# Kernel optimization log

Hardware: AMD Instinct MI355X
Metric: run time of the kernel (lower is better)

Reference implementation:

```python
import jax, jax.numpy as jnp
import numpy as np

N, HID, EDGE_DIM, E = 512, 16, 8, 8192
H4 = HID * 4


def _mlp(x, params):
    W0, b0, W1, b1, W2, b2, W3, b3 = params
    h = jax.nn.relu(x @ W0 + b0)
    h = jax.nn.relu(h @ W1 + b1)
    h = jax.nn.relu(h @ W2 + b2)
    return h @ W3 + b3


def setup_inputs() -> dict:
    key = jax.random.key(0)
    ks = jax.random.split(key, 16)
    rng = np.random.default_rng(0)
    flat = rng.choice(N * N, size=E, replace=False)  # unique edges -> add == set
    edge_index = jnp.asarray(np.stack([flat // N, flat % N]), dtype=jnp.int32)

    def lin(k, fan_in, fan_out):
        kw, kb = jax.random.split(k)
        s = 1.0 / np.sqrt(fan_in)
        return (jax.random.uniform(kw, (fan_in, fan_out), jnp.float32, -s, s),
                jax.random.uniform(kb, (fan_out,), jnp.float32, -s, s))

    W0, b0 = lin(ks[0], EDGE_DIM, H4)
    W1, b1 = lin(ks[1], H4, H4)
    W2, b2 = lin(ks[2], H4, H4)
    W3, b3 = lin(ks[3], H4, HID * HID)
    V0, c0 = lin(ks[4], HID, H4)
    V1, c1 = lin(ks[5], H4, H4)
    V2, c2 = lin(ks[6], H4, H4)
    V3, c3 = lin(ks[7], H4, HID)
    L, Lb = lin(ks[8], HID, HID)

    return {
        'mtr': jax.random.normal(ks[9], (N, N, HID), jnp.float32),
        'edge_attr': jax.random.normal(ks[10], (E, EDGE_DIM), jnp.float32),
        'edge_index': edge_index,
        'W0': W0, 'b0': b0, 'W1': W1, 'b1': b1, 'W2': W2, 'b2': b2, 'W3': W3, 'b3': b3,
        'V0': V0, 'c0': c0, 'V1': V1, 'c1': c1, 'V2': V2, 'c2': c2, 'V3': V3, 'c3': c3,
        'L': L, 'Lb': Lb,
    }


def reference(mtr, edge_attr, edge_index,
              W0, b0, W1, b1, W2, b2, W3, b3,
              V0, c0, V1, c1, V2, c2, V3, c3,
              L, Lb):
    n, hid = mtr.shape[0], mtr.shape[2]
    src, dst = edge_index[0], edge_index[1]
    # per-edge hid x hid matrices (edge_fc)
    F = _mlp(edge_attr, (W0, b0, W1, b1, W2, b2, W3, b3)).reshape(-1, hid, hid)
    # sparse form of einsum('ijc,jkct->ikt', mtr, fmtr): gather src column,
    # per-edge matmul, scatter-add into dst column (edges unique -> == dense set)
    msg = jnp.einsum('iec,ect->iet', mtr[:, src, :], F)          # [n, E, hid]
    mtr1 = jax.ops.segment_sum(msg.transpose(1, 0, 2), dst, num_segments=n)  # [k, i, t]
    mtr1 = mtr1.transpose(1, 0, 2)                                # [i, k, t]
    idx = jnp.arange(n)
    mtr1 = mtr1.at[idx, idx, :].set(0.0)
    mtr1 = mtr1 / hid
    trans = mtr1.transpose(1, 0, 2) @ L + Lb                      # linear(mtr1^T)
    return mtr + _mlp(mtr1 + trans, (V0, c0, V1, c1, V2, c2, V3, c3))
```

## Files before the change

kernel.cpp:

```cpp
#include <hip/hip_runtime.h>
#include <hip/hip_bf16.h>

#define NN 512
#define EE 8192

#define OFF_F     0u
#define OFF_MTR1  2097152u
#define OFF_W     6291456u
#define WR_W0   0
#define WR_B0   512
#define WR_W1   576
#define WR_B1   4672
#define WR_W2   4736
#define WR_B2   8832
#define WR_W3   8896
#define WR_B3   25280
#define WR_V0T  25536
#define WR_C0   26560
#define WR_V1   26624
#define WR_C1   30720
#define WR_V2   30784
#define WR_C2   34880
#define WR_V3   34944
#define WR_C3   35968
#define WR_L    35984
#define WR_LB   36240
#define W_TOTAL 36256
#define OFF_OFFS    (OFF_W + W_TOTAL)
#define OFF_SORTED  (OFF_OFFS + 513)
#define OFF_FLAG    (OFF_SORTED + EE)
#define OFF_MTRT    6336420u
#define OFF_OFFSP   8433572u
#define OFF_SORTEDP 8434085u
#define OFF_FPACK   8442792u
#define OFF_VPACK   9491496u
#define WS_NEED_BYTES  ((size_t)(OFF_MTRT  + 2097152u) * 4u)
#define WS_FULL_BYTES  ((size_t)(OFF_FPACK + 1048704u) * 4u)
#define WS_FULL2_BYTES ((size_t)(OFF_VPACK + 5632u) * 4u)

#define VP0OFF 0
#define VP1OFF 2048
#define VP2OFF 6144
#define VP3OFF 10240

#define XSTR 72
#define RSTR 20

typedef __attribute__((ext_vector_type(8))) short bf16x8;
typedef __attribute__((ext_vector_type(4))) float f32x4;

__device__ __forceinline__ float bflo(unsigned u){ return __uint_as_float(u << 16); }
__device__ __forceinline__ float bfhi(unsigned u){ return __uint_as_float(u & 0xffff0000u); }
__device__ __forceinline__ unsigned short f2bf(float f){
  __hip_bfloat16 h = __float2bfloat16(f);
  union { __hip_bfloat16 hh; unsigned short ss; } u;
  u.hh = h; return u.ss;
}
__device__ __forceinline__ unsigned pack2(float a, float b){
  return (unsigned)f2bf(a) | ((unsigned)f2bf(b) << 16);
}

__device__ __forceinline__ void load16f(const void* base, size_t eoff, int f32, float m[16]) {
  if (f32) {
    const float4* p = (const float4*)((const float*)base + eoff);
    float4 a = p[0], b = p[1], c = p[2], d = p[3];
    m[0]=a.x; m[1]=a.y; m[2]=a.z; m[3]=a.w;
    m[4]=b.x; m[5]=b.y; m[6]=b.z; m[7]=b.w;
    m[8]=c.x; m[9]=c.y; m[10]=c.z; m[11]=c.w;
    m[12]=d.x; m[13]=d.y; m[14]=d.z; m[15]=d.w;
  } else {
    const uint4* p = (const uint4*)((const __hip_bfloat16*)base + eoff);
    uint4 u0 = p[0], u1 = p[1];
    m[0]=bflo(u0.x);  m[1]=bfhi(u0.x);  m[2]=bflo(u0.y);  m[3]=bfhi(u0.y);
    m[4]=bflo(u0.z);  m[5]=bfhi(u0.z);  m[6]=bflo(u0.w);  m[7]=bfhi(u0.w);
    m[8]=bflo(u1.x);  m[9]=bfhi(u1.x);  m[10]=bflo(u1.y); m[11]=bfhi(u1.y);
    m[12]=bflo(u1.z); m[13]=bfhi(u1.z); m[14]=bflo(u1.w); m[15]=bfhi(u1.w);
  }
}

__device__ __forceinline__ float ldelem(const void* p, int idx, int f32) {
  return f32 ? ((const float*)p)[idx]
             : __bfloat162float(((const __hip_bfloat16*)p)[idx]);
}

__global__ void prep_weights(
  const void* __restrict__ W0, const void* __restrict__ b0,
  const void* __restrict__ W1, const void* __restrict__ b1,
  const void* __restrict__ W2, const void* __restrict__ b2,
  const void* __restrict__ W3, const void* __restrict__ b3,
  const void* __restrict__ V0, const void* __restrict__ c0,
  const void* __restrict__ V1, const void* __restrict__ c1,
  const void* __restrict__ V2, const void* __restrict__ c2,
  const void* __restrict__ V3, const void* __restrict__ c3,
  const void* __restrict__ L,  const void* __restrict__ Lb,
  const unsigned short* __restrict__ mtr_u16,
  int* __restrict__ flag, float* __restrict__ w)
{
  __shared__ float mx[256];
  int tid = threadIdx.x;
  float m = 0.f;
  for (int t = tid; t < 4096; t += 256) {
    float v = __uint_as_float(((unsigned)mtr_u16[t]) << 16);
    if (v != v) m = 3e38f;
    else m = fmaxf(m, fabsf(v));
  }
  mx[tid] = m;
  __syncthreads();
  for (int s = 128; s > 0; s >>= 1) {
    if (tid < s) mx[tid] = fmaxf(mx[tid], mx[tid + s]);
    __syncthreads();
  }
  const int f32 = (mx[0] > 1e6f) ? 1 : 0;
  if (blockIdx.x == 0 && tid == 0) flag[0] = f32;

  int g = blockIdx.x * blockDim.x + tid;
  int stride = gridDim.x * blockDim.x;
  auto cv = [&](const void* p, int off, int n){
    for (int i = g; i < n; i += stride) w[off + i] = ldelem(p, i, f32);
  };
  cv(W0, WR_W0, 512);  cv(b0, WR_B0, 64);
  cv(W1, WR_W1, 4096); cv(b1, WR_B1, 64);
  cv(W2, WR_W2, 4096); cv(b2, WR_B2, 64);
  cv(W3, WR_W3, 16384);cv(b3, WR_B3, 256);
  for (int idx = g; idx < 1024; idx += stride) {
    int j = idx >> 4, t = idx & 15;
    w[WR_V0T + idx] = ldelem(V0, t * 64 + j, f32);
  }
  cv(c0, WR_C0, 64);
  cv(V1, WR_V1, 4096); cv(c1, WR_C1, 64);
  cv(V2, WR_V2, 4096); cv(c2, WR_C2, 64);
  cv(V3, WR_V3, 1024); cv(c3, WR_C3, 16);
  cv(L,  WR_L,  256);  cv(Lb, WR_LB, 16);
}

__global__ void prep_vpack(const float* __restrict__ w, unsigned short* __restrict__ VP)
{
  int g = blockIdx.x * blockDim.x + threadIdx.x;
  int stride = gridDim.x * blockDim.x;
  for (int idx = g; idx < 2048; idx += stride) {
    int j = idx & 7, lp = (idx >> 3) & 63, nt = idx >> 9;
    int nn = lp & 15, qq = lp >> 4;
    int kk = qq * 8 + j;
    float v = (kk < 16) ? w[WR_V0T + (nt * 16 + nn) * 16 + kk] : 0.f;
    VP[VP0OFF + idx] = f2bf(v);
  }
  for (int idx = g; idx < 4096; idx += stride) {
    int j = idx & 7, lp = (idx >> 3) & 63, tile = idx >> 9;
    int nn = lp & 15, qq = lp >> 4;
    int kc = tile >> 2, nt = tile & 3;
    int kk = kc * 32 + qq * 8 + j;
    VP[VP1OFF + idx] = f2bf(w[WR_V1 + kk * 64 + nt * 16 + nn]);
    VP[VP2OFF + idx] = f2bf(w[WR_V2 + kk * 64 + nt * 16 + nn]);
  }
  for (int idx = g; idx < 1024; idx += stride) {
    int j = idx & 7, lp = (idx >> 3) & 63, kc = idx >> 9;
    int nn = lp & 15, qq = lp >> 4;
    int kk = kc * 32 + qq * 8 + j;
    VP[VP3OFF + idx] = f2bf(w[WR_V3 + kk * 16 + nn]);
  }
}

__global__ void build_bins(const int* __restrict__ ei,
                           int* __restrict__ offs, int* __restrict__ sorted,
                           int* __restrict__ offsP, int* __restrict__ sortedP,
                           unsigned short* __restrict__ Fpack, int write_pack)
{
  __shared__ int cnt[512];
  __shared__ int pcs[512];
  __shared__ int cur[512];
  __shared__ int curP[512];
  int tid = threadIdx.x;
  cnt[tid] = 0;
  __syncthreads();
  for (int e = tid; e < EE; e += 512) atomicAdd(&cnt[ei[EE + e]], 1);
  __syncthreads();
  int myc = cnt[tid];
  int myp = (myc + 1) & ~1;
  pcs[tid] = myp;
  __syncthreads();
  for (int off = 1; off < 512; off <<= 1) {
    int a = 0, b = 0;
    if (tid >= off) { a = cnt[tid - off]; b = pcs[tid - off]; }
    __syncthreads();
    cnt[tid] += a; pcs[tid] += b;
    __syncthreads();
  }
  int exc  = cnt[tid] - myc;
  int excP = pcs[tid] - myp;
  offs[tid]  = exc;
  offsP[tid] = excP;
  if (tid == 511) { offs[512] = cnt[511]; offsP[512] = pcs[511]; }
  cur[tid]  = exc;
  curP[tid] = excP;
  if (myc & 1) sortedP[excP + myc] = EE;
  __syncthreads();
  for (int e = tid; e < EE; e += 512) {
    int d = ei[EE + e];
    sorted[atomicAdd(&cur[d], 1)]   = e;
    sortedP[atomicAdd(&curP[d], 1)] = e;
  }
  if (write_pack) {
    unsigned* fz = (unsigned*)(Fpack + (size_t)EE * 256);
    for (int idx = tid; idx < 128; idx += 512) fz[idx] = 0u;
  }
}

__global__ __launch_bounds__(256) void transpose_mtr(
  const void* __restrict__ mtr, const int* __restrict__ flag,
  __hip_bfloat16* __restrict__ mtrT)
{
  const int f32 = flag[0];
  int s = blockIdx.x;
  int i = blockIdx.y * 256 + threadIdx.x;
  float m[16];
  load16f(mtr, (size_t)i * 8192 + (size_t)s * 16, f32, m);
  unsigned pw[8];
  #pragma unroll
  for (int q = 0; q < 8; q++) pw[q] = pack2(m[2*q], m[2*q+1]);
  uint4* op = (uint4*)(mtrT + (size_t)s * 8192 + (size_t)i * 16);
  op[0] = make_uint4(pw[0], pw[1], pw[2], pw[3]);
  op[1] = make_uint4(pw[4], pw[5], pw[6], pw[7]);
}

__global__ __launch_bounds__(256) void edge_mlp(
  const void* __restrict__ ea, const float* __restrict__ w,
  const int* __restrict__ flag, float* __restrict__ Fws,
  unsigned short* __restrict__ Fpack, int write_pack)
{
  const int f32 = flag[0];
  const float* W0f = w + WR_W0; const float* b0f = w + WR_B0;
  const float* W1f = w + WR_W1; const float* b1f = w + WR_B1;
  const float* W2f = w + WR_W2; const float* b2f = w + WR_B2;
  const float* W3f = w + WR_W3; const float* b3f = w + WR_B3;
  int tid = threadIdx.x;
  int eg = tid >> 6, lane = tid & 63;
  int e = blockIdx.x * 4 + eg;
  __shared__ float shA[4][64];
  __shared__ float shB[4][64];

  float x[8];
  if (f32) {
    const float4* p = (const float4*)((const float*)ea + (size_t)e * 8);
    float4 a = p[0], b = p[1];
    x[0]=a.x; x[1]=a.y; x[2]=a.z; x[3]=a.w;
    x[4]=b.x; x[5]=b.y; x[6]=b.z; x[7]=b.w;
  } else {
    uint4 u = *(const uint4*)((const __hip_bfloat16*)ea + (size_t)e * 8);
    x[0]=bflo(u.x); x[1]=bfhi(u.x); x[2]=bflo(u.y); x[3]=bfhi(u.y);
    x[4]=bflo(u.z); x[5]=bfhi(u.z); x[6]=bflo(u.w); x[7]=bfhi(u.w);
  }

  float s = b0f[lane];
  #pragma unroll
  for (int c = 0; c < 8; c++) s += x[c] * W0f[c * 64 + lane];
  shA[eg][lane] = fmaxf(s, 0.f);
  __syncthreads();

  s = b1f[lane];
  #pragma unroll
  for (int c = 0; c < 64; c++) s += shA[eg][c] * W1f[c * 64 + lane];
  shB[eg][lane] = fmaxf(s, 0.f);
  __syncthreads();

  s = b2f[lane];
  #pragma unroll
  for (int c = 0; c < 64; c++) s += shB[eg][c] * W2f[c * 64 + lane];
  shA[eg][lane] = fmaxf(s, 0.f);
  __syncthreads();

  int quad = lane >> 4, tt = lane & 15;
  #pragma unroll
  for (int r = 0; r < 4; r++) {
    int o = r * 64 + lane;
    float t = b3f[o];
    #pragma unroll
    for (int c = 0; c < 64; c++) t += shA[eg][c] * W3f[c * 256 + o];
    Fws[(size_t)e * 256 + o] = t;
    if (write_pack) {
      int cc = r * 4 + quad;
      Fpack[(size_t)e * 256 + (cc >> 3) * 128 + tt * 8 + (cc & 7)] = f2bf(t);
    }
  }
}

__global__ __launch_bounds__(256) void message_mfma(
  const __hip_bfloat16* __restrict__ mtrT, const int* __restrict__ ei,
  const unsigned short* __restrict__ Fpack, const int* __restrict__ offsP,
  const int* __restrict__ sortedP, float* __restrict__ mtr1T)
{
  int k = blockIdx.x;
  int tid = threadIdx.x;
  int wave = tid >> 6, lane = tid & 63;
  int n = lane & 15, quad = lane >> 4;
  int qh = quad >> 1;
  int qq = quad & 1;
  int ibase = blockIdx.y * 256 + wave * 64;
  int j0 = offsP[k], j1 = offsP[k + 1];

  f32x4 acc[4];
  #pragma unroll
  for (int mt = 0; mt < 4; mt++) acc[mt] = (f32x4){0.f, 0.f, 0.f, 0.f};

  for (int j = j0; j < j1; j += 2) {
    int e1 = __builtin_amdgcn_readfirstlane(sortedP[j]);
    int e2 = __builtin_amdgcn_readfirstlane(sortedP[j + 1]);
    int s1 = __builtin_amdgcn_readfirstlane(ei[e1]);
    int s2 = (e2 < EE) ? __builtin_amdgcn_readfirstlane(ei[e2]) : 0;
    int es = qh ? e2 : e1;
    int ss = qh ? s2 : s1;
    bf16x8 bfrag = *(const bf16x8*)(Fpack + (size_t)es * 256 + (qq * 16 + n) * 8);
    const __hip_bfloat16* abase = mtrT + (size_t)ss * 8192 + qq * 8;
    #pragma unroll
    for (int mt = 0; mt < 4; mt++) {
      int i = ibase + mt * 16 + n;
      bf16x8 afrag = *(const bf16x8*)(abase + (size_t)i * 16);
      acc[mt] = __builtin_amdgcn_mfma_f32_16x16x32_bf16(afrag, bfrag, acc[mt], 0, 0, 0);
    }
  }

  float* obase = mtr1T + (size_t)k * 8192;
  #pragma unroll
  for (int mt = 0; mt < 4; mt++) {
    int irow = ibase + mt * 16 + quad * 4;
    #pragma unroll
    for (int reg = 0; reg < 4; reg++)
      obase[(size_t)(irow + reg) * 16 + n] = acc[mt][reg];
  }
}

__global__ __launch_bounds__(256) void message_kernel_t(
  const __hip_bfloat16* __restrict__ mtrT, const int* __restrict__ ei,
  const float* __restrict__ Fws, const int* __restrict__ offs,
  const int* __restrict__ sorted, float* __restrict__ mtr1T)
{
  int k = blockIdx.x;
  int i = blockIdx.y * 256 + threadIdx.x;
  float acc[16];
  #pragma unroll
  for (int t = 0; t < 16; t++) acc[t] = 0.f;
  int j0 = offs[k], j1 = offs[k + 1];
  for (int j = j0; j < j1; j++) {
    int e = __builtin_amdgcn_readfirstlane(sorted[j]);
    int s = __builtin_amdgcn_readfirstlane(ei[e]);
    float m[16];
    load16f(mtrT, (size_t)s * 8192 + (size_t)i * 16, 0, m);
    const float4* Fe = (const float4*)(Fws + (size_t)e * 256);
    #pragma unroll
    for (int c = 0; c < 16; c++) {
      float4 f0 = Fe[c*4+0], f1 = Fe[c*4+1], f2 = Fe[c*4+2], f3 = Fe[c*4+3];
      acc[0]  += m[c]*f0.x; acc[1]  += m[c]*f0.y; acc[2]  += m[c]*f0.z; acc[3]  += m[c]*f0.w;
      acc[4]  += m[c]*f1.x; acc[5]  += m[c]*f1.y; acc[6]  += m[c]*f1.z; acc[7]  += m[c]*f1.w;
      acc[8]  += m[c]*f2.x; acc[9]  += m[c]*f2.y; acc[10] += m[c]*f2.z; acc[11] += m[c]*f2.w;
      acc[12] += m[c]*f3.x; acc[13] += m[c]*f3.y; acc[14] += m[c]*f3.z; acc[15] += m[c]*f3.w;
    }
  }
  float4* op = (float4*)(mtr1T + (size_t)k * 8192 + (size_t)i * 16);
  op[0] = make_float4(acc[0],  acc[1],  acc[2],  acc[3]);
  op[1] = make_float4(acc[4],  acc[5],  acc[6],  acc[7]);
  op[2] = make_float4(acc[8],  acc[9],  acc[10], acc[11]);
  op[3] = make_float4(acc[12], acc[13], acc[14], acc[15]);
}

__global__ __launch_bounds__(256) void message_kernel_direct(
  const void* __restrict__ mtr, const int* __restrict__ ei,
  const float* __restrict__ Fws, const int* __restrict__ offs,
  const int* __restrict__ sorted, const int* __restrict__ flag,
  float* __restrict__ mtr1T)
{
  const int f32 = flag[0];
  int k = blockIdx.x;
  int i = blockIdx.y * 256 + threadIdx.x;
  float acc[16];
  #pragma unroll
  for (int t = 0; t < 16; t++) acc[t] = 0.f;
  int j0 = offs[k], j1 = offs[k + 1];
  for (int j = j0; j < j1; j++) {
    int e = __builtin_amdgcn_readfirstlane(sorted[j]);
    int s = __builtin_amdgcn_readfirstlane(ei[e]);
    float m[16];
    load16f(mtr, (size_t)i * 8192 + s * 16, f32, m);
    const float4* Fe = (const float4*)(Fws + (size_t)e * 256);
    #pragma unroll
    for (int c = 0; c < 16; c++) {
      float4 f0 = Fe[c*4+0], f1 = Fe[c*4+1], f2 = Fe[c*4+2], f3 = Fe[c*4+3];
      acc[0]  += m[c]*f0.x; acc[1]  += m[c]*f0.y; acc[2]  += m[c]*f0.z; acc[3]  += m[c]*f0.w;
      acc[4]  += m[c]*f1.x; acc[5]  += m[c]*f1.y; acc[6]  += m[c]*f1.z; acc[7]  += m[c]*f1.w;
      acc[8]  += m[c]*f2.x; acc[9]  += m[c]*f2.y; acc[10] += m[c]*f2.z; acc[11] += m[c]*f2.w;
      acc[12] += m[c]*f3.x; acc[13] += m[c]*f3.y; acc[14] += m[c]*f3.z; acc[15] += m[c]*f3.w;
    }
  }
  float4* op = (float4*)(mtr1T + (size_t)k * 8192 + i * 16);
  op[0] = make_float4(acc[0],  acc[1],  acc[2],  acc[3]);
  op[1] = make_float4(acc[4],  acc[5],  acc[6],  acc[7]);
  op[2] = make_float4(acc[8],  acc[9],  acc[10], acc[11]);
  op[3] = make_float4(acc[12], acc[13], acc[14], acc[15]);
}

__global__ __launch_bounds__(256, 4) void final_mfma(
  const void* __restrict__ mtr, const float* __restrict__ w,
  const float* __restrict__ mtr1T, const int* __restrict__ flag,
  const unsigned short* __restrict__ VP, void* __restrict__ out)
{
  const int f32 = flag[0];
  __shared__ __attribute__((aligned(16))) unsigned short XB[256 * XSTR];
  int tid = threadIdx.x;
  int ti = blockIdx.x >> 5, tk = blockIdx.x & 31;
  int r = tid >> 4, c = tid & 15;
  int i = ti * 16 + r, k = tk * 16 + c;
  float scale = (i == k) ? 0.f : 0.0625f;

  float y[16];
  {
    float a[16], b[16];
    const float4* pa = (const float4*)(mtr1T + (size_t)k * 8192 + (size_t)i * 16);
    const float4* pb = (const float4*)(mtr1T + (size_t)i * 8192 + (size_t)k * 16);
    #pragma unroll
    for (int q4 = 0; q4 < 4; q4++) {
      float4 va = pa[q4], vb = pb[q4];
      a[q4*4+0]=va.x*scale; a[q4*4+1]=va.y*scale; a[q4*4+2]=va.z*scale; a[q4*4+3]=va.w*scale;
      b[q4*4+0]=vb.x*scale; b[q4*4+1]=vb.y*scale; b[q4*4+2]=vb.z*scale; b[q4*4+3]=vb.w*scale;
    }
    const float* Lf  = w + WR_L;
    const float* Lbf = w + WR_LB;
    #pragma unroll
    for (int t = 0; t < 16; t++) y[t] = a[t] + Lbf[t];
    #pragma unroll
    for (int cc = 0; cc < 16; cc++) {
      #pragma unroll
      for (int t = 0; t < 16; t++) y[t] += b[cc] * Lf[cc * 16 + t];
    }
  }
  {
    uint4* row = (uint4*)(XB + tid * XSTR);
    row[0] = make_uint4(pack2(y[0],y[1]),  pack2(y[2],y[3]),
                        pack2(y[4],y[5]),  pack2(y[6],y[7]));
    row[1] = make_uint4(pack2(y[8],y[9]),  pack2(y[10],y[11]),
                        pack2(y[12],y[13]),pack2(y[14],y[15]));
    row[2] = make_uint4(0,0,0,0);
    row[3] = make_uint4(0,0,0,0);
  }

  int wave = tid >> 6, lane = tid & 63;
  int m15 = lane & 15, q = lane >> 4;
  int mtb = wave * 4;

  {
    bf16x8 af[4];
    #pragma unroll
    for (int t4 = 0; t4 < 4; t4++)
      af[t4] = *(const bf16x8*)(XB + ((mtb + t4) * 16 + m15) * XSTR + q * 8);
    #pragma unroll
    for (int nt = 0; nt < 4; nt++) {
      bf16x8 bf_ = *(const bf16x8*)(VP + VP0OFF + nt * 512 + (q * 16 + m15) * 8);
      float bias = w[WR_C0 + nt * 16 + m15];
      #pragma unroll
      for (int t4 = 0; t4 < 4; t4++) {
        f32x4 acc = (f32x4){0.f,0.f,0.f,0.f};
        acc = __builtin_amdgcn_mfma_f32_16x16x32_bf16(af[t4], bf_, acc, 0, 0, 0);
        int pbase = (mtb + t4) * 16 + q * 4;
        #pragma unroll
        for (int reg = 0; reg < 4; reg++)
          XB[(pbase + reg) * XSTR + nt * 16 + m15] = f2bf(fmaxf(acc[reg] + bias, 0.f));
      }
    }
  }
  #pragma unroll
  for (int layer = 0; layer < 2; layer++) {
    int vpo  = layer ? VP2OFF : VP1OFF;
    int wrc  = layer ? WR_C2  : WR_C1;
    bf16x8 af[8];
    #pragma unroll
    for (int t4 = 0; t4 < 4; t4++) {
      #pragma unroll
      for (int kc = 0; kc < 2; kc++)
        af[t4*2+kc] = *(const bf16x8*)(XB + ((mtb + t4) * 16 + m15) * XSTR + kc * 32 + q * 8);
    }
    #pragma unroll
    for (int nt = 0; nt < 4; nt++) {
      bf16x8 b0 = *(const bf16x8*)(VP + vpo + (0 * 4 + nt) * 512 + (q * 16 + m15) * 8);
      bf16x8 b1 = *(const bf16x8*)(VP + vpo + (1 * 4 + nt) * 512 + (q * 16 + m15) * 8);
      float bias = w[wrc + nt * 16 + m15];
      #pragma unroll
      for (int t4 = 0; t4 < 4; t4++) {
        f32x4 acc = (f32x4){0.f,0.f,0.f,0.f};
        acc = __builtin_amdgcn_mfma_f32_16x16x32_bf16(af[t4*2+0], b0, acc, 0, 0, 0);
        acc = __builtin_amdgcn_mfma_f32_16x16x32_bf16(af[t4*2+1], b1, acc, 0, 0, 0);
        int pbase = (mtb + t4) * 16 + q * 4;
        #pragma unroll
        for (int reg = 0; reg < 4; reg++)
          XB[(pbase + reg) * XSTR + nt * 16 + m15] = f2bf(fmaxf(acc[reg] + bias, 0.f));
      }
    }
  }
  f32x4 acc4[4];
  float bias4;
  {
    bf16x8 af[8];
    #pragma unroll
    for (int t4 = 0; t4 < 4; t4++) {
      #pragma unroll
      for (int kc = 0; kc < 2; kc++)
        af[t4*2+kc] = *(const bf16x8*)(XB + ((mtb + t4) * 16 + m15) * XSTR + kc * 32 + q * 8);
    }
    bf16x8 b0 = *(const bf16x8*)(VP + VP3OFF + 0 * 512 + (q * 16 + m15) * 8);
    bf16x8 b1 = *(const bf16x8*)(VP + VP3OFF + 1 * 512 + (q * 16 + m15) * 8);
    bias4 = w[WR_C3 + m15];
    #pragma unroll
    for (int t4 = 0; t4 < 4; t4++) {
      f32x4 acc = (f32x4){0.f,0.f,0.f,0.f};
      acc = __builtin_amdgcn_mfma_f32_16x16x32_bf16(af[t4*2+0], b0, acc, 0, 0, 0);
      acc = __builtin_amdgcn_mfma_f32_16x16x32_bf16(af[t4*2+1], b1, acc, 0, 0, 0);
      acc4[t4] = acc;
    }
  }
  __syncthreads();
  float* RRB = (float*)XB;
  #pragma unroll
  for (int t4 = 0; t4 < 4; t4++) {
    int pbase = (mtb + t4) * 16 + q * 4;
    #pragma unroll
    for (int reg = 0; reg < 4; reg++)
      RRB[(pbase + reg) * RSTR + m15] = acc4[t4][reg] + bias4;
  }
  float rr[16];
  {
    const float4* rp = (const float4*)(RRB + tid * RSTR);
    float4 v0 = rp[0], v1 = rp[1], v2 = rp[2], v3 = rp[3];
    rr[0]=v0.x; rr[1]=v0.y; rr[2]=v0.z; rr[3]=v0.w;
    rr[4]=v1.x; rr[5]=v1.y; rr[6]=v1.z; rr[7]=v1.w;
    rr[8]=v2.x; rr[9]=v2.y; rr[10]=v2.z; rr[11]=v2.w;
    rr[12]=v3.x; rr[13]=v3.y; rr[14]=v3.z; rr[15]=v3.w;
  }
  size_t base = (size_t)i * 8192 + (size_t)k * 16;
  float mv[16];
  load16f(mtr, base, f32, mv);
  if (f32) {
    float4* op = (float4*)((float*)out + base);
    op[0] = make_float4(mv[0]+rr[0],  mv[1]+rr[1],  mv[2]+rr[2],  mv[3]+rr[3]);
    op[1] = make_float4(mv[4]+rr[4],  mv[5]+rr[5],  mv[6]+rr[6],  mv[7]+rr[7]);
    op[2] = make_float4(mv[8]+rr[8],  mv[9]+rr[9],  mv[10]+rr[10],mv[11]+rr[11]);
    op[3] = make_float4(mv[12]+rr[12],mv[13]+rr[13],mv[14]+rr[14],mv[15]+rr[15]);
  } else {
    unsigned pw[8];
    #pragma unroll
    for (int q2 = 0; q2 < 8; q2++)
      pw[q2] = pack2(mv[2*q2] + rr[2*q2], mv[2*q2+1] + rr[2*q2+1]);
    uint4* op = (uint4*)((__hip_bfloat16*)out + base);
    op[0] = make_uint4(pw[0], pw[1], pw[2], pw[3]);
    op[1] = make_uint4(pw[4], pw[5], pw[6], pw[7]);
  }
}

__global__ __launch_bounds__(256, 4) void final_kernel(
  const void* __restrict__ mtr, const float* __restrict__ w,
  const float* __restrict__ mtr1T, const int* __restrict__ flag,
  void* __restrict__ out)
{
  const int f32 = flag[0];
  __shared__ unsigned hbuf[32 * 256];
  int tid = threadIdx.x;
  int ti = blockIdx.x >> 5, tk = blockIdx.x & 31;
  int r = tid >> 4, c = tid & 15;
  int i = ti * 16 + r, k = tk * 16 + c;
  float scale = (i == k) ? 0.f : 0.0625f;

  float y[16];
  {
    float a[16], b[16];
    const float4* pa = (const float4*)(mtr1T + (size_t)k * 8192 + (size_t)i * 16);
    const float4* pb = (const float4*)(mtr1T + (size_t)i * 8192 + (size_t)k * 16);
    #pragma unroll
    for (int q = 0; q < 4; q++) {
      float4 va = pa[q], vb = pb[q];
      a[q*4+0]=va.x*scale; a[q*4+1]=va.y*scale; a[q*4+2]=va.z*scale; a[q*4+3]=va.w*scale;
      b[q*4+0]=vb.x*scale; b[q*4+1]=vb.y*scale; b[q*4+2]=vb.z*scale; b[q*4+3]=vb.w*scale;
    }
    const float* Lf  = w + WR_L;
    const float* Lbf = w + WR_LB;
    #pragma unroll
    for (int t = 0; t < 16; t++) y[t] = a[t] + Lbf[t];
    #pragma unroll
    for (int cc = 0; cc < 16; cc++) {
      #pragma unroll
      for (int t = 0; t < 16; t++) y[t] += b[cc] * Lf[cc * 16 + t];
    }
  }
  {
    const float* V0t = w + WR_V0T; const float* c0f = w + WR_C0;
    for (int m = 0; m < 32; m++) {
      float s0 = c0f[2*m], s1 = c0f[2*m+1];
      #pragma unroll
      for (int t = 0; t < 16; t++) {
        s0 += y[t] * V0t[(2*m) * 16 + t];
        s1 += y[t] * V0t[(2*m+1) * 16 + t];
      }
      hbuf[m * 256 + tid] = pack2(fmaxf(s0, 0.f), fmaxf(s1, 0.f));
    }
  }
  #pragma unroll
  for (int lyr = 0; lyr < 2; lyr++) {
    const float* Vf = w + (lyr ? WR_V2 : WR_V1);
    const float* cf = w + (lyr ? WR_C2 : WR_C1);
    unsigned held[16];
    #pragma unroll
    for (int pass = 0; pass < 2; pass++) {
      float s[32];
      #pragma unroll
      for (int jj = 0; jj < 32; jj++) s[jj] = cf[pass * 32 + jj];
      for (int m = 0; m < 32; m++) {
        unsigned hu = hbuf[m * 256 + tid];
        float h0 = bflo(hu), h1 = bfhi(hu);
        #pragma unroll
        for (int jj = 0; jj < 32; jj++)
          s[jj] += h0 * Vf[(2*m) * 64 + pass*32 + jj] + h1 * Vf[(2*m+1) * 64 + pass*32 + jj];
      }
      if (pass == 0) {
        #pragma unroll
        for (int q = 0; q < 16; q++) held[q] = pack2(fmaxf(s[2*q], 0.f), fmaxf(s[2*q+1], 0.f));
      } else {
        #pragma unroll
        for (int q = 0; q < 16; q++) hbuf[q * 256 + tid] = held[q];
        #pragma unroll
        for (int q = 0; q < 16; q++) hbuf[(16 + q) * 256 + tid] = pack2(fmaxf(s[2*q], 0.f), fmaxf(s[2*q+1], 0.f));
      }
    }
  }
  float rr[16];
  {
    const float* V3f = w + WR_V3; const float* c3f = w + WR_C3;
    #pragma unroll
    for (int t = 0; t < 16; t++) rr[t] = c3f[t];
    for (int m = 0; m < 32; m++) {
      unsigned hu = hbuf[m * 256 + tid];
      float h0 = bflo(hu), h1 = bfhi(hu);
      #pragma unroll
      for (int t = 0; t < 16; t++)
        rr[t] += h0 * V3f[(2*m) * 16 + t] + h1 * V3f[(2*m+1) * 16 + t];
    }
  }
  size_t base = (size_t)i * 8192 + (size_t)k * 16;
  float mv[16];
  load16f(mtr, base, f32, mv);
  if (f32) {
    float4* op = (float4*)((float*)out + base);
    op[0] = make_float4(mv[0]+rr[0],  mv[1]+rr[1],  mv[2]+rr[2],  mv[3]+rr[3]);
    op[1] = make_float4(mv[4]+rr[4],  mv[5]+rr[5],  mv[6]+rr[6],  mv[7]+rr[7]);
    op[2] = make_float4(mv[8]+rr[8],  mv[9]+rr[9],  mv[10]+rr[10],mv[11]+rr[11]);
    op[3] = make_float4(mv[12]+rr[12],mv[13]+rr[13],mv[14]+rr[14],mv[15]+rr[15]);
  } else {
    unsigned pw[8];
    #pragma unroll
    for (int q = 0; q < 8; q++)
      pw[q] = pack2(mv[2*q] + rr[2*q], mv[2*q+1] + rr[2*q+1]);
    uint4* op = (uint4*)((__hip_bfloat16*)out + base);
    op[0] = make_uint4(pw[0], pw[1], pw[2], pw[3]);
    op[1] = make_uint4(pw[4], pw[5], pw[6], pw[7]);
  }
}

extern "C" void kernel_launch(void* const* d_in, const int* in_sizes, int n_in,
                              void* d_out, int out_size, void* d_ws, size_t ws_size,
                              hipStream_t stream)
{
  const void* mtr = d_in[0];
  const void* ea  = d_in[1];
  const int*  ei  = (const int*)d_in[2];

  float* ws    = (float*)d_ws;
  float* Fws   = ws + OFF_F;
  float* mtr1T = ws + OFF_MTR1;
  float* w     = ws + OFF_W;
  int* offs    = (int*)(ws + OFF_OFFS);
  int* sorted  = (int*)(ws + OFF_SORTED);
  int* flag    = (int*)(ws + OFF_FLAG);
  __hip_bfloat16* mtrT = (__hip_bfloat16*)(ws + OFF_MTRT);
  int* offsP   = (int*)(ws + OFF_OFFSP);
  int* sortedP = (int*)(ws + OFF_SORTEDP);
  unsigned short* Fpack = (unsigned short*)(ws + OFF_FPACK);
  unsigned short* VP    = (unsigned short*)(ws + OFF_VPACK);

  int full2 = ws_size >= WS_FULL2_BYTES;
  int full  = ws_size >= WS_FULL_BYTES;
  int mid   = ws_size >= WS_NEED_BYTES;

  prep_weights<<<32, 256, 0, stream>>>(d_in[3], d_in[4], d_in[5], d_in[6],
                                       d_in[7], d_in[8], d_in[9], d_in[10],
                                       d_in[11], d_in[12], d_in[13], d_in[14],
                                       d_in[15], d_in[16], d_in[17], d_in[18],
                                       d_in[19], d_in[20],
                                       (const unsigned short*)mtr, flag, w);
  if (full2) prep_vpack<<<8, 256, 0, stream>>>(w, VP);
  build_bins<<<1, 512, 0, stream>>>(ei, offs, sorted, offsP, sortedP, Fpack, full);
  edge_mlp<<<EE / 4, 256, 0, stream>>>(ea, w, flag, Fws, Fpack, full);

  dim3 gmsg(512, 2);
  if (full) {
    transpose_mtr<<<gmsg, 256, 0, stream>>>(mtr, flag, mtrT);
    message_mfma<<<gmsg, 256, 0, stream>>>(mtrT, ei, Fpack, offsP, sortedP, mtr1T);
  } else if (mid) {
    transpose_mtr<<<gmsg, 256, 0, stream>>>(mtr, flag, mtrT);
    message_kernel_t<<<gmsg, 256, 0, stream>>>(mtrT, ei, Fws, offs, sorted, mtr1T);
  } else {
    message_kernel_direct<<<gmsg, 256, 0, stream>>>(mtr, ei, Fws, offs, sorted, flag, mtr1T);
  }
  if (full2)
    final_mfma<<<1024, 256, 0, stream>>>(mtr, w, mtr1T, flag, VP, d_out);
  else
    final_kernel<<<1024, 256, 0, stream>>>(mtr, w, mtr1T, flag, d_out);
}
```

Before: 221.0 us.

## Fuse prep, binning, transpose and edge MLP into one launch; pack src into bins

Merges the weight conversion, V packing, edge binning, mtr transpose and edge MLP into a single heterogeneous prep_all kernel. Each block detects the dtype itself and reads the raw inputs directly. Bins now store the edge id and source index packed together, so the message kernel no longer does a dependent lookup into edge_index. The goal is to cut kernel launch overheads and serial dependencies between the small prep stages. The cost is that every block repeats the dtype-detection reduction, and the edge MLP blocks read raw weights instead of the converted copies.

```diff
diff --git a/kernel.cpp b/kernel.cpp
--- a/kernel.cpp
+++ b/kernel.cpp
@@ -31,11 +31,10 @@
 #define OFF_FLAG    (OFF_SORTED + EE)
 #define OFF_MTRT    6336420u
 #define OFF_OFFSP   8433572u
-#define OFF_SORTEDP 8434085u
+#define OFF_PACKP   8434085u
 #define OFF_FPACK   8442792u
 #define OFF_VPACK   9491496u
 #define WS_NEED_BYTES  ((size_t)(OFF_MTRT  + 2097152u) * 4u)
-#define WS_FULL_BYTES  ((size_t)(OFF_FPACK + 1048704u) * 4u)
 #define WS_FULL2_BYTES ((size_t)(OFF_VPACK + 5632u) * 4u)
 
 #define VP0OFF 0
@@ -59,6 +58,8 @@
 __device__ __forceinline__ unsigned pack2(float a, float b){
   return (unsigned)f2bf(a) | ((unsigned)f2bf(b) << 16);
 }
+__device__ __forceinline__ float cvt(float v){ return v; }
+__device__ __forceinline__ float cvt(__hip_bfloat16 v){ return __bfloat162float(v); }
 
 __device__ __forceinline__ void load16f(const void* base, size_t eoff, int f32, float m[16]) {
   if (f32) {
@@ -83,6 +84,403 @@
              : __bfloat162float(((const __hip_bfloat16*)p)[idx]);
 }
 
+__device__ __forceinline__ int detect_f32_local(const unsigned short* mtr_u16, float* red) {
+  int tid = threadIdx.x;
+  float m = 0.f;
+  for (int t = tid; t < 4096; t += 512) {
+    float v = __uint_as_float(((unsigned)mtr_u16[t]) << 16);
+    if (v != v) m = 3e38f;
+    else m = fmaxf(m, fabsf(v));
+  }
+  red[tid] = m;
+  __syncthreads();
+  for (int s = 256; s > 0; s >>= 1) {
+    if (tid < s) red[tid] = fmaxf(red[tid], red[tid + s]);
+    __syncthreads();
+  }
+  float mx = red[0];
+  __syncthreads();
+  return (mx > 1e6f) ? 1 : 0;
+}
+
+template <typename T>
+__device__ void edge_body(const T* __restrict__ ea,
+                          const T* __restrict__ W0, const T* __restrict__ b0,
+                          const T* __restrict__ W1, const T* __restrict__ b1,
+                          const T* __restrict__ W2, const T* __restrict__ b2,
+                          const T* __restrict__ W3, const T* __restrict__ b3,
+                          int e, int eg, int lane,
+                          float (*shA)[64], float (*shB)[64],
+                          unsigned short* __restrict__ Fpack)
+{
+  float x[8];
+  #pragma unroll
+  for (int c = 0; c < 8; c++) x[c] = cvt(ea[(size_t)e * 8 + c]);
+
+  float s = cvt(b0[lane]);
+  #pragma unroll
+  for (int c = 0; c < 8; c++) s += x[c] * cvt(W0[c * 64 + lane]);
+  shA[eg][lane] = fmaxf(s, 0.f);
+  __syncthreads();
+
+  s = cvt(b1[lane]);
+  #pragma unroll
+  for (int c = 0; c < 64; c++) s += shA[eg][c] * cvt(W1[c * 64 + lane]);
+  shB[eg][lane] = fmaxf(s, 0.f);
+  __syncthreads();
+
+  s = cvt(b2[lane]);
+  #pragma unroll
+  for (int c = 0; c < 64; c++) s += shB[eg][c] * cvt(W2[c * 64 + lane]);
+  shA[eg][lane] = fmaxf(s, 0.f);
+  __syncthreads();
+
+  int quad = lane >> 4, tt = lane & 15;
+  #pragma unroll
+  for (int r = 0; r < 4; r++) {
+    int o = r * 64 + lane;
+    float t = cvt(b3[o]);
+    #pragma unroll
+    for (int c = 0; c < 64; c++) t += shA[eg][c] * cvt(W3[c * 256 + o]);
+    int cc = r * 4 + quad;
+    Fpack[(size_t)e * 256 + (cc >> 3) * 128 + tt * 8 + (cc & 7)] = f2bf(t);
+  }
+}
+
+__global__ __launch_bounds__(512) void prep_all(
+  const void* __restrict__ mtr, const void* __restrict__ ea, const int* __restrict__ ei,
+  const void* __restrict__ W0, const void* __restrict__ b0,
+  const void* __restrict__ W1, const void* __restrict__ b1,
+  const void* __restrict__ W2, const void* __restrict__ b2,
+  const void* __restrict__ W3, const void* __restrict__ b3,
+  const void* __restrict__ V0, const void* __restrict__ c0,
+  const void* __restrict__ V1, const void* __restrict__ c1,
+  const void* __restrict__ V2, const void* __restrict__ c2,
+  const void* __restrict__ V3, const void* __restrict__ c3,
+  const void* __restrict__ L,  const void* __restrict__ Lb,
+  int* __restrict__ flag, float* __restrict__ w, unsigned short* __restrict__ VP,
+  int* __restrict__ offsP, unsigned* __restrict__ packP,
+  unsigned short* __restrict__ Fpack, __hip_bfloat16* __restrict__ mtrT)
+{
+  __shared__ __attribute__((aligned(16))) char smem_raw[8192];
+  int tid = threadIdx.x;
+  int bid = blockIdx.x;
+  const int f32 = detect_f32_local((const unsigned short*)mtr, (float*)smem_raw);
+
+  if (bid == 0) {
+    int* cnt  = (int*)smem_raw;
+    int* pcs  = cnt + 512;
+    int* curP = pcs + 512;
+    cnt[tid] = 0;
+    if (tid == 0) flag[0] = f32;
+    __syncthreads();
+    for (int e = tid; e < EE; e += 512) atomicAdd(&cnt[ei[EE + e]], 1);
+    __syncthreads();
+    int myc = cnt[tid];
+    int myp = (myc + 1) & ~1;
+    pcs[tid] = myp;
+    __syncthreads();
+    for (int off = 1; off < 512; off <<= 1) {
+      int b = (tid >= off) ? pcs[tid - off] : 0;
+      __syncthreads();
+      pcs[tid] += b;
+      __syncthreads();
+    }
+    int excP = pcs[tid] - myp;
+    offsP[tid] = excP;
+    if (tid == 511) offsP[512] = pcs[511];
+    curP[tid] = excP;
+    if (myc & 1) packP[excP + myc] = EE;
+    __syncthreads();
+    for (int e = tid; e < EE; e += 512) {
+      int d = ei[EE + e];
+      int s = ei[e];
+      packP[atomicAdd(&curP[d], 1)] = (unsigned)e | ((unsigned)s << 14);
+    }
+    unsigned* fz = (unsigned*)(Fpack + (size_t)EE * 256);
+    for (int i2 = tid; i2 < 128; i2 += 512) fz[i2] = 0u;
+  } else if (bid < 33) {
+    int g = (bid - 1) * 512 + tid;
+    const int stride = 32 * 512;
+    auto cv = [&](const void* p, int off, int n){
+      for (int i = g; i < n; i += stride) w[off + i] = ldelem(p, i, f32);
+    };
+    cv(W0, WR_W0, 512);  cv(b0, WR_B0, 64);
+    cv(W1, WR_W1, 4096); cv(b1, WR_B1, 64);
+    cv(W2, WR_W2, 4096); cv(b2, WR_B2, 64);
+    cv(W3, WR_W3, 16384);cv(b3, WR_B3, 256);
+    for (int idx = g; idx < 1024; idx += stride) {
+      int j = idx >> 4, t = idx & 15;
+      w[WR_V0T + idx] = ldelem(V0, t * 64 + j, f32);
+    }
+    cv(c0, WR_C0, 64);
+    cv(V1, WR_V1, 4096); cv(c1, WR_C1, 64);
+    cv(V2, WR_V2, 4096); cv(c2, WR_C2, 64);
+    cv(V3, WR_V3, 1024); cv(c3, WR_C3, 16);
+    cv(L,  WR_L,  256);  cv(Lb, WR_LB, 16);
+  } else if (bid < 37) {
+    int g = (bid - 33) * 512 + tid;
+    const int stride = 4 * 512;
+    for (int idx = g; idx < 2048; idx += stride) {
+      int j = idx & 7, lp = (idx >> 3) & 63, nt = idx >> 9;
+      int nn = lp & 15, qq = lp >> 4;
+      int kk = qq * 8 + j;
+      float v = (kk < 16) ? ldelem(V0, kk * 64 + nt * 16 + nn, f32) : 0.f;
+      VP[VP0OFF + idx] = f2bf(v);
+    }
+    for (int idx = g; idx < 4096; idx += stride) {
+      int j = idx & 7, lp = (idx >> 3) & 63, tile = idx >> 9;
+      int nn = lp & 15, qq = lp >> 4;
+      int kc = tile >> 2, nt = tile & 3;
+      int kk = kc * 32 + qq * 8 + j;
+      VP[VP1OFF + idx] = f2bf(ldelem(V1, kk * 64 + nt * 16 + nn, f32));
+      VP[VP2OFF + idx] = f2bf(ldelem(V2, kk * 64 + nt * 16 + nn, f32));
+    }
+    for (int idx = g; idx < 1024; idx += stride) {
+      int j = idx & 7, lp = (idx >> 3) & 63, kc = idx >> 9;
+      int nn = lp & 15, qq = lp >> 4;
+      int kk = kc * 32 + qq * 8 + j;
+      VP[VP3OFF + idx] = f2bf(ldelem(V3, kk * 16 + nn, f32));
+    }
+  } else if (bid < 549) {
+    int s = bid - 37;
+    int i = tid;
+    float m[16];
+    load16f(mtr, (size_t)i * 8192 + (size_t)s * 16, f32, m);
+    unsigned pw[8];
+    #pragma unroll
+    for (int q = 0; q < 8; q++) pw[q] = pack2(m[2*q], m[2*q+1]);
+    uint4* op = (uint4*)(mtrT + (size_t)s * 8192 + (size_t)i * 16);
+    op[0] = make_uint4(pw[0], pw[1], pw[2], pw[3]);
+    op[1] = make_uint4(pw[4], pw[5], pw[6], pw[7]);
+  } else {
+    int eg = tid >> 6, lane = tid & 63;
+    int e = (bid - 549) * 8 + eg;
+    float (*shA)[64] = (float(*)[64])smem_raw;
+    float (*shB)[64] = (float(*)[64])(smem_raw + 2048);
+    if (f32)
+      edge_body<float>((const float*)ea,
+        (const float*)W0, (const float*)b0, (const float*)W1, (const float*)b1,
+        (const float*)W2, (const float*)b2, (const float*)W3, (const float*)b3,
+        e, eg, lane, shA, shB, Fpack);
+    else
+      edge_body<__hip_bfloat16>((const __hip_bfloat16*)ea,
+        (const __hip_bfloat16*)W0, (const __hip_bfloat16*)b0,
+        (const __hip_bfloat16*)W1, (const __hip_bfloat16*)b1,
+        (const __hip_bfloat16*)W2, (const __hip_bfloat16*)b2,
+        (const __hip_bfloat16*)W3, (const __hip_bfloat16*)b3,
+        e, eg, lane, shA, shB, Fpack);
+  }
+}
+
+__global__ __launch_bounds__(256) void message_mfma2(
+  const __hip_bfloat16* __restrict__ mtrT,
+  const unsigned short* __restrict__ Fpack,
+  const int* __restrict__ offsP, const unsigned* __restrict__ packP,
+  float* __restrict__ mtr1T)
+{
+  int k = blockIdx.x;
+  int tid = threadIdx.x;
+  int wave = tid >> 6, lane = tid & 63;
+  int n = lane & 15, quad = lane >> 4;
+  int qh = quad >> 1, qq = quad & 1;
+  int ibase = blockIdx.y * 256 + wave * 64;
+  int j0 = offsP[k], j1 = offsP[k + 1];
+
+  f32x4 acc[4];
+  #pragma unroll
+  for (int mt = 0; mt < 4; mt++) acc[mt] = (f32x4){0.f, 0.f, 0.f, 0.f};
+
+  bf16x8 bfrag;
+  bf16x8 af0, af1, af2, af3;
+  auto loadfr = [&](int j) {
+    unsigned p1 = __builtin_amdgcn_readfirstlane(packP[j]);
+    unsigned p2 = __builtin_amdgcn_readfirstlane(packP[j + 1]);
+    unsigned pv = qh ? p2 : p1;
+    int es = (int)(pv & 0x3FFFu);
+    int ss = (int)(pv >> 14);
+    bfrag = *(const bf16x8*)(Fpack + (size_t)es * 256 + (qq * 16 + n) * 8);
+    const __hip_bfloat16* ab = mtrT + (size_t)ss * 8192 + qq * 8;
+    af0 = *(const bf16x8*)(ab + (size_t)(ibase + 0 * 16 + n) * 16);
+    af1 = *(const bf16x8*)(ab + (size_t)(ibase + 1 * 16 + n) * 16);
+    af2 = *(const bf16x8*)(ab + (size_t)(ibase + 2 * 16 + n) * 16);
+    af3 = *(const bf16x8*)(ab + (size_t)(ibase + 3 * 16 + n) * 16);
+  };
+  if (j0 < j1) loadfr(j0);
+  for (int j = j0; j < j1; j += 2) {
+    bf16x8 bc = bfrag, a0 = af0, a1 = af1, a2 = af2, a3 = af3;
+    if (j + 2 < j1) loadfr(j + 2);
+    acc[0] = __builtin_amdgcn_mfma_f32_16x16x32_bf16(a0, bc, acc[0], 0, 0, 0);
+    acc[1] = __builtin_amdgcn_mfma_f32_16x16x32_bf16(a1, bc, acc[1], 0, 0, 0);
+    acc[2] = __builtin_amdgcn_mfma_f32_16x16x32_bf16(a2, bc, acc[2], 0, 0, 0);
+    acc[3] = __builtin_amdgcn_mfma_f32_16x16x32_bf16(a3, bc, acc[3], 0, 0, 0);
+  }
+
+  float* obase = mtr1T + (size_t)k * 8192;
+  #pragma unroll
+  for (int mt = 0; mt < 4; mt++) {
+    int irow = ibase + mt * 16 + quad * 4;
+    #pragma unroll
+    for (int reg = 0; reg < 4; reg++)
+      obase[(size_t)(irow + reg) * 16 + n] = acc[mt][reg];
+  }
+}
+
+__global__ __launch_bounds__(256, 4) void final_mfma(
+  const void* __restrict__ mtr, const float* __restrict__ w,
+  const float* __restrict__ mtr1T, const int* __restrict__ flag,
+  const unsigned short* __restrict__ VP, void* __restrict__ out)
+{
+  const int f32 = flag[0];
+  __shared__ __attribute__((aligned(16))) unsigned short XB[256 * XSTR];
+  int tid = threadIdx.x;
+  int ti = blockIdx.x >> 5, tk = blockIdx.x & 31;
+  int r = tid >> 4, c = tid & 15;
+  int i = ti * 16 + r, k = tk * 16 + c;
+  float scale = (i == k) ? 0.f : 0.0625f;
+
+  float y[16];
+  {
+    float a[16], b[16];
+    const float4* pa = (const float4*)(mtr1T + (size_t)k * 8192 + (size_t)i * 16);
+    const float4* pb = (const float4*)(mtr1T + (size_t)i * 8192 + (size_t)k * 16);
+    #pragma unroll
+    for (int q4 = 0; q4 < 4; q4++) {
+      float4 va = pa[q4], vb = pb[q4];
+      a[q4*4+0]=va.x*scale; a[q4*4+1]=va.y*scale; a[q4*4+2]=va.z*scale; a[q4*4+3]=va.w*scale;
+      b[q4*4+0]=vb.x*scale; b[q4*4+1]=vb.y*scale; b[q4*4+2]=vb.z*scale; b[q4*4+3]=vb.w*scale;
+    }
+    const float* Lf  = w + WR_L;
+    const float* Lbf = w + WR_LB;
+    #pragma unroll
+    for (int t = 0; t < 16; t++) y[t] = a[t] + Lbf[t];
+    #pragma unroll
+    for (int cc = 0; cc < 16; cc++) {
+      #pragma unroll
+      for (int t = 0; t < 16; t++) y[t] += b[cc] * Lf[cc * 16 + t];
+    }
+  }
+  {
+    uint4* row = (uint4*)(XB + tid * XSTR);
+    row[0] = make_uint4(pack2(y[0],y[1]),  pack2(y[2],y[3]),
+                        pack2(y[4],y[5]),  pack2(y[6],y[7]));
+    row[1] = make_uint4(pack2(y[8],y[9]),  pack2(y[10],y[11]),
+                        pack2(y[12],y[13]),pack2(y[14],y[15]));
+    row[2] = make_uint4(0,0,0,0);
+    row[3] = make_uint4(0,0,0,0);
+  }
+
+  int wave = tid >> 6, lane = tid & 63;
+  int m15 = lane & 15, q = lane >> 4;
+  int mtb = wave * 4;
+
+  {
+    bf16x8 af[4];
+    #pragma unroll
+    for (int t4 = 0; t4 < 4; t4++)
+      af[t4] = *(const bf16x8*)(XB + ((mtb + t4) * 16 + m15) * XSTR + q * 8);
+    #pragma unroll
+    for (int nt = 0; nt < 4; nt++) {
+      bf16x8 bf_ = *(const bf16x8*)(VP + VP0OFF + nt * 512 + (q * 16 + m15) * 8);
+      float bias = w[WR_C0 + nt * 16 + m15];
+      #pragma unroll
+      for (int t4 = 0; t4 < 4; t4++) {
+        f32x4 acc = (f32x4){0.f,0.f,0.f,0.f};
+        acc = __builtin_amdgcn_mfma_f32_16x16x32_bf16(af[t4], bf_, acc, 0, 0, 0);
+        int pbase = (mtb + t4) * 16 + q * 4;
+        #pragma unroll
+        for (int reg = 0; reg < 4; reg++)
+          XB[(pbase + reg) * XSTR + nt * 16 + m15] = f2bf(fmaxf(acc[reg] + bias, 0.f));
+      }
+    }
+  }
+  #pragma unroll
+  for (int layer = 0; layer < 2; layer++) {
+    int vpo  = layer ? VP2OFF : VP1OFF;
+    int wrc  = layer ? WR_C2  : WR_C1;
+    bf16x8 af[8];
+    #pragma unroll
+    for (int t4 = 0; t4 < 4; t4++) {
+      #pragma unroll
+      for (int kc = 0; kc < 2; kc++)
+        af[t4*2+kc] = *(const bf16x8*)(XB + ((mtb + t4) * 16 + m15) * XSTR + kc * 32 + q * 8);
+    }
+    #pragma unroll
+    for (int nt = 0; nt < 4; nt++) {
+      bf16x8 b0 = *(const bf16x8*)(VP + vpo + (0 * 4 + nt) * 512 + (q * 16 + m15) * 8);
+      bf16x8 b1 = *(const bf16x8*)(VP + vpo + (1 * 4 + nt) * 512 + (q * 16 + m15) * 8);
+      float bias = w[wrc + nt * 16 + m15];
+      #pragma unroll
+      for (int t4 = 0; t4 < 4; t4++) {
+        f32x4 acc = (f32x4){0.f,0.f,0.f,0.f};
+        acc = __builtin_amdgcn_mfma_f32_16x16x32_bf16(af[t4*2+0], b0, acc, 0, 0, 0);
+        acc = __builtin_amdgcn_mfma_f32_16x16x32_bf16(af[t4*2+1], b1, acc, 0, 0, 0);
+        int pbase = (mtb + t4) * 16 + q * 4;
+        #pragma unroll
+        for (int reg = 0; reg < 4; reg++)
+          XB[(pbase + reg) * XSTR + nt * 16 + m15] = f2bf(fmaxf(acc[reg] + bias, 0.f));
+      }
+    }
+  }
+  f32x4 acc4[4];
+  float bias4;
+  {
+    bf16x8 af[8];
+    #pragma unroll
+    for (int t4 = 0; t4 < 4; t4++) {
+      #pragma unroll
+      for (int kc = 0; kc < 2; kc++)
+        af[t4*2+kc] = *(const bf16x8*)(XB + ((mtb + t4) * 16 + m15) * XSTR + kc * 32 + q * 8);
+    }
+    bf16x8 b0 = *(const bf16x8*)(VP + VP3OFF + 0 * 512 + (q * 16 + m15) * 8);
+    bf16x8 b1 = *(const bf16x8*)(VP + VP3OFF + 1 * 512 + (q * 16 + m15) * 8);
+    bias4 = w[WR_C3 + m15];
+    #pragma unroll
+    for (int t4 = 0; t4 < 4; t4++) {
+      f32x4 acc = (f32x4){0.f,0.f,0.f,0.f};
+      acc = __builtin_amdgcn_mfma_f32_16x16x32_bf16(af[t4*2+0], b0, acc, 0, 0, 0);
+      acc = __builtin_amdgcn_mfma_f32_16x16x32_bf16(af[t4*2+1], b1, acc, 0, 0, 0);
+      acc4[t4] = acc;
+    }
+  }
+  __syncthreads();
+  float* RRB = (float*)XB;
+  #pragma unroll
+  for (int t4 = 0; t4 < 4; t4++) {
+    int pbase = (mtb + t4) * 16 + q * 4;
+    #pragma unroll
+    for (int reg = 0; reg < 4; reg++)
+      RRB[(pbase + reg) * RSTR + m15] = acc4[t4][reg] + bias4;
+  }
+  float rr[16];
+  {
+    const float4* rp = (const float4*)(RRB + tid * RSTR);
+    float4 v0 = rp[0], v1 = rp[1], v2 = rp[2], v3 = rp[3];
+    rr[0]=v0.x; rr[1]=v0.y; rr[2]=v0.z; rr[3]=v0.w;
+    rr[4]=v1.x; rr[5]=v1.y; rr[6]=v1.z; rr[7]=v1.w;
+    rr[8]=v2.x; rr[9]=v2.y; rr[10]=v2.z; rr[11]=v2.w;
+    rr[12]=v3.x; rr[13]=v3.y; rr[14]=v3.z; rr[15]=v3.w;
+  }
+  size_t base = (size_t)i * 8192 + (size_t)k * 16;
+  float mv[16];
+  load16f(mtr, base, f32, mv);
+  if (f32) {
+    float4* op = (float4*)((float*)out + base);
+    op[0] = make_float4(mv[0]+rr[0],  mv[1]+rr[1],  mv[2]+rr[2],  mv[3]+rr[3]);
+    op[1] = make_float4(mv[4]+rr[4],  mv[5]+rr[5],  mv[6]+rr[6],  mv[7]+rr[7]);
+    op[2] = make_float4(mv[8]+rr[8],  mv[9]+rr[9],  mv[10]+rr[10],mv[11]+rr[11]);
+    op[3] = make_float4(mv[12]+rr[12],mv[13]+rr[13],mv[14]+rr[14],mv[15]+rr[15]);
+  } else {
+    unsigned pw[8];
+    #pragma unroll
+    for (int q2 = 0; q2 < 8; q2++)
+      pw[q2] = pack2(mv[2*q2] + rr[2*q2], mv[2*q2+1] + rr[2*q2+1]);
+    uint4* op = (uint4*)((__hip_bfloat16*)out + base);
+    op[0] = make_uint4(pw[0], pw[1], pw[2], pw[3]);
+    op[1] = make_uint4(pw[4], pw[5], pw[6], pw[7]);
+  }
+}
+
 __global__ void prep_weights(
   const void* __restrict__ W0, const void* __restrict__ b0,
   const void* __restrict__ W1, const void* __restrict__ b1,
@@ -133,99 +531,37 @@
   cv(L,  WR_L,  256);  cv(Lb, WR_LB, 16);
 }
 
-__global__ void prep_vpack(const float* __restrict__ w, unsigned short* __restrict__ VP)
-{
-  int g = blockIdx.x * blockDim.x + threadIdx.x;
-  int stride = gridDim.x * blockDim.x;
-  for (int idx = g; idx < 2048; idx += stride) {
-    int j = idx & 7, lp = (idx >> 3) & 63, nt = idx >> 9;
-    int nn = lp & 15, qq = lp >> 4;
-    int kk = qq * 8 + j;
-    float v = (kk < 16) ? w[WR_V0T + (nt * 16 + nn) * 16 + kk] : 0.f;
-    VP[VP0OFF + idx] = f2bf(v);
-  }
-  for (int idx = g; idx < 4096; idx += stride) {
-    int j = idx & 7, lp = (idx >> 3) & 63, tile = idx >> 9;
-    int nn = lp & 15, qq = lp >> 4;
-    int kc = tile >> 2, nt = tile & 3;
-    int kk = kc * 32 + qq * 8 + j;
-    VP[VP1OFF + idx] = f2bf(w[WR_V1 + kk * 64 + nt * 16 + nn]);
-    VP[VP2OFF + idx] = f2bf(w[WR_V2 + kk * 64 + nt * 16 + nn]);
-  }
-  for (int idx = g; idx < 1024; idx += stride) {
-    int j = idx & 7, lp = (idx >> 3) & 63, kc = idx >> 9;
-    int nn = lp & 15, qq = lp >> 4;
-    int kk = kc * 32 + qq * 8 + j;
-    VP[VP3OFF + idx] = f2bf(w[WR_V3 + kk * 16 + nn]);
-  }
-}
-
-__global__ void build_bins(const int* __restrict__ ei,
-                           int* __restrict__ offs, int* __restrict__ sorted,
-                           int* __restrict__ offsP, int* __restrict__ sortedP,
-                           unsigned short* __restrict__ Fpack, int write_pack)
+__global__ void build_bins_basic(const int* __restrict__ ei,
+                                 int* __restrict__ offs, int* __restrict__ sorted)
 {
   __shared__ int cnt[512];
-  __shared__ int pcs[512];
   __shared__ int cur[512];
-  __shared__ int curP[512];
   int tid = threadIdx.x;
   cnt[tid] = 0;
   __syncthreads();
   for (int e = tid; e < EE; e += 512) atomicAdd(&cnt[ei[EE + e]], 1);
   __syncthreads();
   int myc = cnt[tid];
-  int myp = (myc + 1) & ~1;
-  pcs[tid] = myp;
-  __syncthreads();
   for (int off = 1; off < 512; off <<= 1) {
-    int a = 0, b = 0;
-    if (tid >= off) { a = cnt[tid - off]; b = pcs[tid - off]; }
+    int add = (tid >= off) ? cnt[tid - off] : 0;
     __syncthreads();
-    cnt[tid] += a; pcs[tid] += b;
+    cnt[tid] += add;
     __syncthreads();
   }
-  int exc  = cnt[tid] - myc;
-  int excP = pcs[tid] - myp;
-  offs[tid]  = exc;
-  offsP[tid] = excP;
-  if (tid == 511) { offs[512] = cnt[511]; offsP[512] = pcs[511]; }
-  cur[tid]  = exc;
-  curP[tid] = excP;
-  if (myc & 1) sortedP[excP + myc] = EE;
+  int excl = cnt[tid] - myc;
+  offs[tid] = excl;
+  if (tid == 511) offs[512] = cnt[511];
+  cur[tid] = excl;
   __syncthreads();
   for (int e = tid; e < EE; e += 512) {
     int d = ei[EE + e];
-    sorted[atomicAdd(&cur[d], 1)]   = e;
-    sortedP[atomicAdd(&curP[d], 1)] = e;
-  }
-  if (write_pack) {
-    unsigned* fz = (unsigned*)(Fpack + (size_t)EE * 256);
-    for (int idx = tid; idx < 128; idx += 512) fz[idx] = 0u;
-  }
-}
-
-__global__ __launch_bounds__(256) void transpose_mtr(
-  const void* __restrict__ mtr, const int* __restrict__ flag,
-  __hip_bfloat16* __restrict__ mtrT)
-{
-  const int f32 = flag[0];
-  int s = blockIdx.x;
-  int i = blockIdx.y * 256 + threadIdx.x;
-  float m[16];
-  load16f(mtr, (size_t)i * 8192 + (size_t)s * 16, f32, m);
-  unsigned pw[8];
-  #pragma unroll
-  for (int q = 0; q < 8; q++) pw[q] = pack2(m[2*q], m[2*q+1]);
-  uint4* op = (uint4*)(mtrT + (size_t)s * 8192 + (size_t)i * 16);
-  op[0] = make_uint4(pw[0], pw[1], pw[2], pw[3]);
-  op[1] = make_uint4(pw[4], pw[5], pw[6], pw[7]);
-}
-
-__global__ __launch_bounds__(256) void edge_mlp(
+    sorted[atomicAdd(&cur[d], 1)] = e;
+  }
+}
+
+__global__ __launch_bounds__(256) void edge_mlp_fb(
   const void* __restrict__ ea, const float* __restrict__ w,
-  const int* __restrict__ flag, float* __restrict__ Fws,
-  unsigned short* __restrict__ Fpack, int write_pack)
+  const int* __restrict__ flag, float* __restrict__ Fws)
 {
   const int f32 = flag[0];
   const float* W0f = w + WR_W0; const float* b0f = w + WR_B0;
@@ -237,128 +573,32 @@
   int e = blockIdx.x * 4 + eg;
   __shared__ float shA[4][64];
   __shared__ float shB[4][64];
-
   float x[8];
-  if (f32) {
-    const float4* p = (const float4*)((const float*)ea + (size_t)e * 8);
-    float4 a = p[0], b = p[1];
-    x[0]=a.x; x[1]=a.y; x[2]=a.z; x[3]=a.w;
-    x[4]=b.x; x[5]=b.y; x[6]=b.z; x[7]=b.w;
-  } else {
-    uint4 u = *(const uint4*)((const __hip_bfloat16*)ea + (size_t)e * 8);
-    x[0]=bflo(u.x); x[1]=bfhi(u.x); x[2]=bflo(u.y); x[3]=bfhi(u.y);
-    x[4]=bflo(u.z); x[5]=bfhi(u.z); x[6]=bflo(u.w); x[7]=bfhi(u.w);
-  }
-
+  #pragma unroll
+  for (int c = 0; c < 8; c++) x[c] = ldelem(ea, e * 8 + c, f32);
   float s = b0f[lane];
   #pragma unroll
   for (int c = 0; c < 8; c++) s += x[c] * W0f[c * 64 + lane];
   shA[eg][lane] = fmaxf(s, 0.f);
   __syncthreads();
-
   s = b1f[lane];
   #pragma unroll
   for (int c = 0; c < 64; c++) s += shA[eg][c] * W1f[c * 64 + lane];
   shB[eg][lane] = fmaxf(s, 0.f);
   __syncthreads();
-
   s = b2f[lane];
   #pragma unroll
   for (int c = 0; c < 64; c++) s += shB[eg][c] * W2f[c * 64 + lane];
   shA[eg][lane] = fmaxf(s, 0.f);
   __syncthreads();
-
-  int quad = lane >> 4, tt = lane & 15;
-  #pragma unroll
-  for (int r = 0; r < 4; r++) {
-    int o = r * 64 + lane;
+  #pragma unroll
+  for (int r2 = 0; r2 < 4; r2++) {
+    int o = r2 * 64 + lane;
     float t = b3f[o];
     #pragma unroll
     for (int c = 0; c < 64; c++) t += shA[eg][c] * W3f[c * 256 + o];
     Fws[(size_t)e * 256 + o] = t;
-    if (write_pack) {
-      int cc = r * 4 + quad;
-      Fpack[(size_t)e * 256 + (cc >> 3) * 128 + tt * 8 + (cc & 7)] = f2bf(t);
-    }
-  }
-}
-
-__global__ __launch_bounds__(256) void message_mfma(
-  const __hip_bfloat16* __restrict__ mtrT, const int* __restrict__ ei,
-  const unsigned short* __restrict__ Fpack, const int* __restrict__ offsP,
-  const int* __restrict__ sortedP, float* __restrict__ mtr1T)
-{
-  int k = blockIdx.x;
-  int tid = threadIdx.x;
-  int wave = tid >> 6, lane = tid & 63;
-  int n = lane & 15, quad = lane >> 4;
-  int qh = quad >> 1;
-  int qq = quad & 1;
-  int ibase = blockIdx.y * 256 + wave * 64;
-  int j0 = offsP[k], j1 = offsP[k + 1];
-
-  f32x4 acc[4];
-  #pragma unroll
-  for (int mt = 0; mt < 4; mt++) acc[mt] = (f32x4){0.f, 0.f, 0.f, 0.f};
-
-  for (int j = j0; j < j1; j += 2) {
-    int e1 = __builtin_amdgcn_readfirstlane(sortedP[j]);
-    int e2 = __builtin_amdgcn_readfirstlane(sortedP[j + 1]);
-    int s1 = __builtin_amdgcn_readfirstlane(ei[e1]);
-    int s2 = (e2 < EE) ? __builtin_amdgcn_readfirstlane(ei[e2]) : 0;
-    int es = qh ? e2 : e1;
-    int ss = qh ? s2 : s1;
-    bf16x8 bfrag = *(const bf16x8*)(Fpack + (size_t)es * 256 + (qq * 16 + n) * 8);
-    const __hip_bfloat16* abase = mtrT + (size_t)ss * 8192 + qq * 8;
-    #pragma unroll
-    for (int mt = 0; mt < 4; mt++) {
-      int i = ibase + mt * 16 + n;
-      bf16x8 afrag = *(const bf16x8*)(abase + (size_t)i * 16);
-      acc[mt] = __builtin_amdgcn_mfma_f32_16x16x32_bf16(afrag, bfrag, acc[mt], 0, 0, 0);
-    }
-  }
-
-  float* obase = mtr1T + (size_t)k * 8192;
-  #pragma unroll
-  for (int mt = 0; mt < 4; mt++) {
-    int irow = ibase + mt * 16 + quad * 4;
-    #pragma unroll
-    for (int reg = 0; reg < 4; reg++)
-      obase[(size_t)(irow + reg) * 16 + n] = acc[mt][reg];
-  }
-}
-
-__global__ __launch_bounds__(256) void message_kernel_t(
-  const __hip_bfloat16* __restrict__ mtrT, const int* __restrict__ ei,
-  const float* __restrict__ Fws, const int* __restrict__ offs,
-  const int* __restrict__ sorted, float* __restrict__ mtr1T)
-{
-  int k = blockIdx.x;
-  int i = blockIdx.y * 256 + threadIdx.x;
-  float acc[16];
-  #pragma unroll
-  for (int t = 0; t < 16; t++) acc[t] = 0.f;
-  int j0 = offs[k], j1 = offs[k + 1];
-  for (int j = j0; j < j1; j++) {
-    int e = __builtin_amdgcn_readfirstlane(sorted[j]);
-    int s = __builtin_amdgcn_readfirstlane(ei[e]);
-    float m[16];
-    load16f(mtrT, (size_t)s * 8192 + (size_t)i * 16, 0, m);
-    const float4* Fe = (const float4*)(Fws + (size_t)e * 256);
-    #pragma unroll
-    for (int c = 0; c < 16; c++) {
-      float4 f0 = Fe[c*4+0], f1 = Fe[c*4+1], f2 = Fe[c*4+2], f3 = Fe[c*4+3];
-      acc[0]  += m[c]*f0.x; acc[1]  += m[c]*f0.y; acc[2]  += m[c]*f0.z; acc[3]  += m[c]*f0.w;
-      acc[4]  += m[c]*f1.x; acc[5]  += m[c]*f1.y; acc[6]  += m[c]*f1.z; acc[7]  += m[c]*f1.w;
-      acc[8]  += m[c]*f2.x; acc[9]  += m[c]*f2.y; acc[10] += m[c]*f2.z; acc[11] += m[c]*f2.w;
-      acc[12] += m[c]*f3.x; acc[13] += m[c]*f3.y; acc[14] += m[c]*f3.z; acc[15] += m[c]*f3.w;
-    }
-  }
-  float4* op = (float4*)(mtr1T + (size_t)k * 8192 + (size_t)i * 16);
-  op[0] = make_float4(acc[0],  acc[1],  acc[2],  acc[3]);
-  op[1] = make_float4(acc[4],  acc[5],  acc[6],  acc[7]);
-  op[2] = make_float4(acc[8],  acc[9],  acc[10], acc[11]);
-  op[3] = make_float4(acc[12], acc[13], acc[14], acc[15]);
+  }
 }
 
 __global__ __launch_bounds__(256) void message_kernel_direct(
@@ -396,162 +636,7 @@
   op[3] = make_float4(acc[12], acc[13], acc[14], acc[15]);
 }
 
-__global__ __launch_bounds__(256, 4) void final_mfma(
-  const void* __restrict__ mtr, const float* __restrict__ w,
-  const float* __restrict__ mtr1T, const int* __restrict__ flag,
-  const unsigned short* __restrict__ VP, void* __restrict__ out)
-{
-  const int f32 = flag[0];
-  __shared__ __attribute__((aligned(16))) unsigned short XB[256 * XSTR];
-  int tid = threadIdx.x;
-  int ti = blockIdx.x >> 5, tk = blockIdx.x & 31;
-  int r = tid >> 4, c = tid & 15;
-  int i = ti * 16 + r, k = tk * 16 + c;
-  float scale = (i == k) ? 0.f : 0.0625f;
-
-  float y[16];
-  {
-    float a[16], b[16];
-    const float4* pa = (const float4*)(mtr1T + (size_t)k * 8192 + (size_t)i * 16);
-    const float4* pb = (const float4*)(mtr1T + (size_t)i * 8192 + (size_t)k * 16);
-    #pragma unroll
-    for (int q4 = 0; q4 < 4; q4++) {
-      float4 va = pa[q4], vb = pb[q4];
-      a[q4*4+0]=va.x*scale; a[q4*4+1]=va.y*scale; a[q4*4+2]=va.z*scale; a[q4*4+3]=va.w*scale;
-      b[q4*4+0]=vb.x*scale; b[q4*4+1]=vb.y*scale; b[q4*4+2]=vb.z*scale; b[q4*4+3]=vb.w*scale;
-    }
-    const float* Lf  = w + WR_L;
-    const float* Lbf = w + WR_LB;
-    #pragma unroll
-    for (int t = 0; t < 16; t++) y[t] = a[t] + Lbf[t];
-    #pragma unroll
-    for (int cc = 0; cc < 16; cc++) {
-      #pragma unroll
-      for (int t = 0; t < 16; t++) y[t] += b[cc] * Lf[cc * 16 + t];
-    }
-  }
-  {
-    uint4* row = (uint4*)(XB + tid * XSTR);
-    row[0] = make_uint4(pack2(y[0],y[1]),  pack2(y[2],y[3]),
-                        pack2(y[4],y[5]),  pack2(y[6],y[7]));
-    row[1] = make_uint4(pack2(y[8],y[9]),  pack2(y[10],y[11]),
-                        pack2(y[12],y[13]),pack2(y[14],y[15]));
-    row[2] = make_uint4(0,0,0,0);
-    row[3] = make_uint4(0,0,0,0);
-  }
-
-  int wave = tid >> 6, lane = tid & 63;
-  int m15 = lane & 15, q = lane >> 4;
-  int mtb = wave * 4;
-
-  {
-    bf16x8 af[4];
-    #pragma unroll
-    for (int t4 = 0; t4 < 4; t4++)
-      af[t4] = *(const bf16x8*)(XB + ((mtb + t4) * 16 + m15) * XSTR + q * 8);
-    #pragma unroll
-    for (int nt = 0; nt < 4; nt++) {
-      bf16x8 bf_ = *(const bf16x8*)(VP + VP0OFF + nt * 512 + (q * 16 + m15) * 8);
-      float bias = w[WR_C0 + nt * 16 + m15];
-      #pragma unroll
-      for (int t4 = 0; t4 < 4; t4++) {
-        f32x4 acc = (f32x4){0.f,0.f,0.f,0.f};
-        acc = __builtin_amdgcn_mfma_f32_16x16x32_bf16(af[t4], bf_, acc, 0, 0, 0);
-        int pbase = (mtb + t4) * 16 + q * 4;
-        #pragma unroll
-        for (int reg = 0; reg < 4; reg++)
-          XB[(pbase + reg) * XSTR + nt * 16 + m15] = f2bf(fmaxf(acc[reg] + bias, 0.f));
-      }
-    }
-  }
-  #pragma unroll
-  for (int layer = 0; layer < 2; layer++) {
-    int vpo  = layer ? VP2OFF : VP1OFF;
-    int wrc  = layer ? WR_C2  : WR_C1;
-    bf16x8 af[8];
-    #pragma unroll
-    for (int t4 = 0; t4 < 4; t4++) {
-      #pragma unroll
-      for (int kc = 0; kc < 2; kc++)
-        af[t4*2+kc] = *(const bf16x8*)(XB + ((mtb + t4) * 16 + m15) * XSTR + kc * 32 + q * 8);
-    }
-    #pragma unroll
-    for (int nt = 0; nt < 4; nt++) {
-      bf16x8 b0 = *(const bf16x8*)(VP + vpo + (0 * 4 + nt) * 512 + (q * 16 + m15) * 8);
-      bf16x8 b1 = *(const bf16x8*)(VP + vpo + (1 * 4 + nt) * 512 + (q * 16 + m15) * 8);
-      float bias = w[wrc + nt * 16 + m15];
-      #pragma unroll
-      for (int t4 = 0; t4 < 4; t4++) {
-        f32x4 acc = (f32x4){0.f,0.f,0.f,0.f};
-        acc = __builtin_amdgcn_mfma_f32_16x16x32_bf16(af[t4*2+0], b0, acc, 0, 0, 0);
-        acc = __builtin_amdgcn_mfma_f32_16x16x32_bf16(af[t4*2+1], b1, acc, 0, 0, 0);
-        int pbase = (mtb + t4) * 16 + q * 4;
-        #pragma unroll
-        for (int reg = 0; reg < 4; reg++)
-          XB[(pbase + reg) * XSTR + nt * 16 + m15] = f2bf(fmaxf(acc[reg] + bias, 0.f));
-      }
-    }
-  }
-  f32x4 acc4[4];
-  float bias4;
-  {
-    bf16x8 af[8];
-    #pragma unroll
-    for (int t4 = 0; t4 < 4; t4++) {
-      #pragma unroll
-      for (int kc = 0; kc < 2; kc++)
-        af[t4*2+kc] = *(const bf16x8*)(XB + ((mtb + t4) * 16 + m15) * XSTR + kc * 32 + q * 8);
-    }
-    bf16x8 b0 = *(const bf16x8*)(VP + VP3OFF + 0 * 512 + (q * 16 + m15) * 8);
-    bf16x8 b1 = *(const bf16x8*)(VP + VP3OFF + 1 * 512 + (q * 16 + m15) * 8);
-    bias4 = w[WR_C3 + m15];
-    #pragma unroll
-    for (int t4 = 0; t4 < 4; t4++) {
-      f32x4 acc = (f32x4){0.f,0.f,0.f,0.f};
-      acc = __builtin_amdgcn_mfma_f32_16x16x32_bf16(af[t4*2+0], b0, acc, 0, 0, 0);
-      acc = __builtin_amdgcn_mfma_f32_16x16x32_bf16(af[t4*2+1], b1, acc, 0, 0, 0);
-      acc4[t4] = acc;
-    }
-  }
-  __syncthreads();
-  float* RRB = (float*)XB;
-  #pragma unroll
-  for (int t4 = 0; t4 < 4; t4++) {
-    int pbase = (mtb + t4) * 16 + q * 4;
-    #pragma unroll
-    for (int reg = 0; reg < 4; reg++)
-      RRB[(pbase + reg) * RSTR + m15] = acc4[t4][reg] + bias4;
-  }
-  float rr[16];
-  {
-    const float4* rp = (const float4*)(RRB + tid * RSTR);
-    float4 v0 = rp[0], v1 = rp[1], v2 = rp[2], v3 = rp[3];
-    rr[0]=v0.x; rr[1]=v0.y; rr[2]=v0.z; rr[3]=v0.w;
-    rr[4]=v1.x; rr[5]=v1.y; rr[6]=v1.z; rr[7]=v1.w;
-    rr[8]=v2.x; rr[9]=v2.y; rr[10]=v2.z; rr[11]=v2.w;
-    rr[12]=v3.x; rr[13]=v3.y; rr[14]=v3.z; rr[15]=v3.w;
-  }
-  size_t base = (size_t)i * 8192 + (size_t)k * 16;
-  float mv[16];
-  load16f(mtr, base, f32, mv);
-  if (f32) {
-    float4* op = (float4*)((float*)out + base);
-    op[0] = make_float4(mv[0]+rr[0],  mv[1]+rr[1],  mv[2]+rr[2],  mv[3]+rr[3]);
-    op[1] = make_float4(mv[4]+rr[4],  mv[5]+rr[5],  mv[6]+rr[6],  mv[7]+rr[7]);
-    op[2] = make_float4(mv[8]+rr[8],  mv[9]+rr[9],  mv[10]+rr[10],mv[11]+rr[11]);
-    op[3] = make_float4(mv[12]+rr[12],mv[13]+rr[13],mv[14]+rr[14],mv[15]+rr[15]);
-  } else {
-    unsigned pw[8];
-    #pragma unroll
-    for (int q2 = 0; q2 < 8; q2++)
-      pw[q2] = pack2(mv[2*q2] + rr[2*q2], mv[2*q2+1] + rr[2*q2+1]);
-    uint4* op = (uint4*)((__hip_bfloat16*)out + base);
-    op[0] = make_uint4(pw[0], pw[1], pw[2], pw[3]);
-    op[1] = make_uint4(pw[4], pw[5], pw[6], pw[7]);
-  }
-}
-
-__global__ __launch_bounds__(256, 4) void final_kernel(
+__global__ __launch_bounds__(256, 4) void final_kernel_fb(
   const void* __restrict__ mtr, const float* __restrict__ w,
   const float* __restrict__ mtr1T, const int* __restrict__ flag,
   void* __restrict__ out)
@@ -563,7 +648,6 @@
   int r = tid >> 4, c = tid & 15;
   int i = ti * 16 + r, k = tk * 16 + c;
   float scale = (i == k) ? 0.f : 0.0625f;
-
   float y[16];
   {
     float a[16], b[16];
@@ -675,36 +759,31 @@
   int* flag    = (int*)(ws + OFF_FLAG);
   __hip_bfloat16* mtrT = (__hip_bfloat16*)(ws + OFF_MTRT);
   int* offsP   = (int*)(ws + OFF_OFFSP);
-  int* sortedP = (int*)(ws + OFF_SORTEDP);
+  unsigned* packP = (unsigned*)(ws + OFF_PACKP);
   unsigned short* Fpack = (unsigned short*)(ws + OFF_FPACK);
   unsigned short* VP    = (unsigned short*)(ws + OFF_VPACK);
 
-  int full2 = ws_size >= WS_FULL2_BYTES;
-  int full  = ws_size >= WS_FULL_BYTES;
-  int mid   = ws_size >= WS_NEED_BYTES;
-
-  prep_weights<<<32, 256, 0, stream>>>(d_in[3], d_in[4], d_in[5], d_in[6],
-                                       d_in[7], d_in[8], d_in[9], d_in[10],
-                                       d_in[11], d_in[12], d_in[13], d_in[14],
-                                       d_in[15], d_in[16], d_in[17], d_in[18],
-                                       d_in[19], d_in[20],
-                                       (const unsigned short*)mtr, flag, w);
-  if (full2) prep_vpack<<<8, 256, 0, stream>>>(w, VP);
-  build_bins<<<1, 512, 0, stream>>>(ei, offs, sorted, offsP, sortedP, Fpack, full);
-  edge_mlp<<<EE / 4, 256, 0, stream>>>(ea, w, flag, Fws, Fpack, full);
-
-  dim3 gmsg(512, 2);
-  if (full) {
-    transpose_mtr<<<gmsg, 256, 0, stream>>>(mtr, flag, mtrT);
-    message_mfma<<<gmsg, 256, 0, stream>>>(mtrT, ei, Fpack, offsP, sortedP, mtr1T);
-  } else if (mid) {
-    transpose_mtr<<<gmsg, 256, 0, stream>>>(mtr, flag, mtrT);
-    message_kernel_t<<<gmsg, 256, 0, stream>>>(mtrT, ei, Fws, offs, sorted, mtr1T);
+  if (ws_size >= WS_FULL2_BYTES) {
+    prep_all<<<1573, 512, 0, stream>>>(
+        mtr, ea, ei,
+        d_in[3], d_in[4], d_in[5], d_in[6], d_in[7], d_in[8], d_in[9], d_in[10],
+        d_in[11], d_in[12], d_in[13], d_in[14], d_in[15], d_in[16], d_in[17], d_in[18],
+        d_in[19], d_in[20],
+        flag, w, VP, offsP, packP, Fpack, mtrT);
+    dim3 gmsg(512, 2);
+    message_mfma2<<<gmsg, 256, 0, stream>>>(mtrT, Fpack, offsP, packP, mtr1T);
+    final_mfma<<<1024, 256, 0, stream>>>(mtr, w, mtr1T, flag, VP, d_out);
   } else {
+    prep_weights<<<32, 256, 0, stream>>>(d_in[3], d_in[4], d_in[5], d_in[6],
+                                         d_in[7], d_in[8], d_in[9], d_in[10],
+                                         d_in[11], d_in[12], d_in[13], d_in[14],
+                                         d_in[15], d_in[16], d_in[17], d_in[18],
+                                         d_in[19], d_in[20],
+                                         (const unsigned short*)mtr, flag, w);
+    build_bins_basic<<<1, 512, 0, stream>>>(ei, offs, sorted);
+    edge_mlp_fb<<<EE / 4, 256, 0, stream>>>(ea, w, flag, Fws);
+    dim3 gmsg(512, 2);
     message_kernel_direct<<<gmsg, 256, 0, stream>>>(mtr, ei, Fws, offs, sorted, flag, mtr1T);
-  }
-  if (full2)
-    final_mfma<<<1024, 256, 0, stream>>>(mtr, w, mtr1T, flag, VP, d_out);
-  else
-    final_kernel<<<1024, 256, 0, stream>>>(mtr, w, mtr1T, flag, d_out);
-}
+    final_kernel_fb<<<1024, 256, 0, stream>>>(mtr, w, mtr1T, flag, d_out);
+  }
+}
```

New measurement: 192.1 us. 13.1% less time.
